# Optimization experiments

Hardware: AMD Instinct MI355X
Metric: run time of the kernel (lower is better)

Reference implementation:

```python
import jax, jax.numpy as jnp
import numpy as np

B, N, F_IN, H, K = 8, 4096, 64, 64, 3


def setup_inputs() -> dict:
    key = jax.random.key(0)
    ks = jax.random.split(key, 8)
    s_in = 1.0 / np.sqrt(F_IN * K)
    s_h = 1.0 / np.sqrt(H * K)
    return {
        "input_tensor": jax.random.normal(ks[0], (B, N, F_IN), jnp.float32),
        "graph": jax.random.normal(ks[1], (B, N, N), jnp.float32) / np.sqrt(N),
        "h_cur": jax.random.normal(ks[2], (B, N, H), jnp.float32),
        "c_cur": jax.random.normal(ks[3], (B, N, H), jnp.float32),
        "W1": jax.random.normal(ks[4], (K, F_IN, 4 * H), jnp.float32) * s_in,
        "b1": jnp.zeros((4 * H,), jnp.float32),
        "W2": jax.random.normal(ks[5], (K, H, 4 * H), jnp.float32) * s_h,
        "b2": jnp.zeros((4 * H,), jnp.float32),
        "batch_size": B,
    }


def cheb_conv(x, L, W, b):
    """Batched Chebyshev graph conv.
    x: [B,N,F], L: [B,N,N] (per-sample scaled Laplacian), W: [K,F,O], b: [O].
    T_0 = x, T_1 = L x, T_k = 2 L T_{k-1} - T_{k-2}; out = sum_k T_k W_k + b.
    """
    k_order = W.shape[0]  # static
    t_km2 = x
    out = jnp.einsum("bnf,fo->bno", t_km2, W[0])
    if k_order > 1:
        t_km1 = jnp.einsum("bmn,bnf->bmf", L, x)
        out = out + jnp.einsum("bnf,fo->bno", t_km1, W[1])
        for k in range(2, k_order):
            t_k = 2.0 * jnp.einsum("bmn,bnf->bmf", L, t_km1) - t_km2
            out = out + jnp.einsum("bnf,fo->bno", t_k, W[k])
            t_km2, t_km1 = t_km1, t_k
    return out + b


def reference(input_tensor, graph, h_cur, c_cur, W1, b1, W2, b2, batch_size):
    # per-sample ChebConv on x and h (batched via einsum), then fused LSTM gates
    combined = cheb_conv(input_tensor, graph, W1, b1) + cheb_conv(h_cur, graph, W2, b2)
    hd = h_cur.shape[-1]
    cc_i, cc_f, cc_o, cc_g = jnp.split(combined, [hd, 2 * hd, 3 * hd], axis=2)
    i = jax.nn.sigmoid(cc_i)
    f = jax.nn.sigmoid(cc_f)
    o = jax.nn.sigmoid(cc_o)
    g = jnp.tanh(cc_g)
    c_next = f * c_cur + i * g
    h_next = o * jnp.tanh(c_next)
    return (h_next, c_next)
```

## Files before the change

kernel.cpp:

```cpp
#include <hip/hip_runtime.h>
#include <stdint.h>

#define BB 8
#define NN 4096
#define HH 64
#define C2 128

typedef float f32x4 __attribute__((ext_vector_type(4)));
typedef __bf16 bf16x8 __attribute__((ext_vector_type(8)));
typedef unsigned int u32x4 __attribute__((ext_vector_type(4)));

__device__ __forceinline__ unsigned short f2bf(float x) {
  unsigned int u = __float_as_uint(x);
  u += 0x7FFFu + ((u >> 16) & 1u);
  return (unsigned short)(u >> 16);
}
__device__ __forceinline__ unsigned int pack2(float a, float b) {
  return (unsigned int)f2bf(a) | ((unsigned int)f2bf(b) << 16);
}

__global__ __launch_bounds__(256) void k_prepX(const float* __restrict__ x,
                                               const float* __restrict__ h,
                                               unsigned short* __restrict__ XbfT) {
  __shared__ __align__(16) unsigned short lds[64 * 136];
  const int b = blockIdx.y;
  const int n0 = blockIdx.x * 64;
  const int t = threadIdx.x;
#pragma unroll
  for (int i = 0; i < 4; ++i) {
    int e = t + i * 256;
    int n = e >> 4, f4 = e & 15;
    size_t src = (((size_t)b * NN + n0 + n) << 6) + f4 * 4;
    f32x4 vx = *(const f32x4*)(x + src);
    f32x4 vh = *(const f32x4*)(h + src);
    unsigned short* px = &lds[n * 136 + f4 * 4];
    px[0] = f2bf(vx.x); px[1] = f2bf(vx.y); px[2] = f2bf(vx.z); px[3] = f2bf(vx.w);
    unsigned short* ph = &lds[n * 136 + 64 + f4 * 4];
    ph[0] = f2bf(vh.x); ph[1] = f2bf(vh.y); ph[2] = f2bf(vh.z); ph[3] = f2bf(vh.w);
  }
  __syncthreads();
  const int f2 = t >> 1, half = t & 1;
  unsigned int w[16];
#pragma unroll
  for (int i = 0; i < 16; ++i) {
    int na = half * 32 + i * 2;
    w[i] = (unsigned int)lds[na * 136 + f2] | ((unsigned int)lds[(na + 1) * 136 + f2] << 16);
  }
  size_t off = ((size_t)b * C2 + f2) * NN + n0 + half * 32;
  u32x4* dst = (u32x4*)(XbfT + off);
  u32x4 v0 = {w[0], w[1], w[2], w[3]};   dst[0] = v0;
  u32x4 v1 = {w[4], w[5], w[6], w[7]};   dst[1] = v1;
  u32x4 v2 = {w[8], w[9], w[10], w[11]}; dst[2] = v2;
  u32x4 v3 = {w[12], w[13], w[14], w[15]}; dst[3] = v3;
}

__global__ __launch_bounds__(256) void k_prepW(const float* __restrict__ W1,
                                               const float* __restrict__ W2,
                                               unsigned short* __restrict__ WcatT) {
  int tid = blockIdx.x * 256 + threadIdx.x;
  int o = tid & 255;
  int kk = (tid >> 8) * 2;
  unsigned int out = 0;
#pragma unroll
  for (int j = 0; j < 2; ++j) {
    int k = kk + j;
    int kb = k >> 6, f = k & 63;
    const float* src = (kb & 1) ? W2 : W1;
    float v = src[(((kb >> 1) * 64 + f) << 8) + o];
    out |= ((unsigned int)f2bf(v)) << (16 * j);
  }
  *(unsigned int*)(WcatT + (size_t)o * 384 + kk) = out;
}

template <int PASS>
__global__ __launch_bounds__(256) void k_gemmL(
    const float* __restrict__ L, const unsigned short* __restrict__ Rt,
    unsigned short* __restrict__ T1row, unsigned short* __restrict__ T1T,
    unsigned short* __restrict__ T2row,
    const float* __restrict__ x, const float* __restrict__ h) {
  __shared__ __align__(16) unsigned short Ab[2][64 * 72];
  __shared__ __align__(16) unsigned short Bbuf[2][128 * 64];
  const int b = blockIdx.y;
  const int n0 = blockIdx.x * 64;
  const int t = threadIdx.x;
  const int w = t >> 6, l = t & 63;
  const int wr = w >> 1, wc = w & 1;
  const int l15 = l & 15, l4 = l >> 4;

  const float* Lb = L + ((size_t)b * NN + n0) * NN;
  const unsigned short* Rb = Rt + (size_t)b * C2 * NN;

  f32x4 areg[2][4];
  u32x4 breg[4];
  f32x4 acc[2][4];
  f32x4 z = {0.f, 0.f, 0.f, 0.f};
#pragma unroll
  for (int i = 0; i < 2; ++i)
#pragma unroll
    for (int j = 0; j < 4; ++j) acc[i][j] = z;

#define LOAD_A(kt, ar)                                                     \
  {                                                                        \
    int k0 = (kt) * 64;                                                    \
    _Pragma("unroll") for (int i = 0; i < 4; ++i) {                        \
      int e = t + i * 256; int row = e >> 4, c4 = e & 15;                  \
      (ar)[i] = *(const f32x4*)(Lb + (size_t)row * NN + k0 + c4 * 4);      \
    }                                                                      \
  }
#define LOAD_B(kt, br)                                                     \
  {                                                                        \
    int k0 = (kt) * 64;                                                    \
    _Pragma("unroll") for (int i = 0; i < 4; ++i) {                        \
      int e = t + i * 256; int c = e >> 3, q = e & 7;                      \
      (br)[i] = *(const u32x4*)(Rb + (size_t)c * NN + k0 + q * 8);         \
    }                                                                      \
  }
#define STORE_A(p, ar)                                                     \
  {                                                                        \
    _Pragma("unroll") for (int i = 0; i < 4; ++i) {                        \
      int e = t + i * 256; int row = e >> 4, c4 = e & 15;                  \
      *(uint2*)&Ab[p][row * 72 + c4 * 4] =                                 \
          make_uint2(pack2((ar)[i].x, (ar)[i].y), pack2((ar)[i].z, (ar)[i].w)); \
    }                                                                      \
  }
#define STORE_B(p, br)                                                     \
  {                                                                        \
    _Pragma("unroll") for (int i = 0; i < 4; ++i) {                        \
      int e = t + i * 256; int c = e >> 3, q = e & 7;                      \
      int ks = (q * 8) ^ ((c & 7) << 3);                                   \
      *(u32x4*)&Bbuf[p][c * 64 + ks] = (br)[i];                            \
    }                                                                      \
  }

  LOAD_A(0, areg[0]);
  LOAD_B(0, breg);
  STORE_A(0, areg[0]);
  STORE_B(0, breg);
  LOAD_A(1, areg[1]);
  __syncthreads();

  const int NT = NN / 64;
  for (int kt = 0; kt < NT; ++kt) {
    const int p = kt & 1;
    if (kt + 2 < NT) LOAD_A(kt + 2, areg[p]);
    if (kt + 1 < NT) LOAD_B(kt + 1, breg);

    bf16x8 af[2][2], bfr[4][2];
#pragma unroll
    for (int rf = 0; rf < 2; ++rf)
#pragma unroll
      for (int ks = 0; ks < 2; ++ks) {
        int n = wr * 32 + rf * 16 + l15;
        af[rf][ks] = *(const bf16x8*)&Ab[p][n * 72 + ks * 32 + l4 * 8];
      }
#pragma unroll
    for (int cf = 0; cf < 4; ++cf)
#pragma unroll
      for (int ks = 0; ks < 2; ++ks) {
        int c = wc * 64 + cf * 16 + l15;
        int kk = (ks * 32 + l4 * 8) ^ ((c & 7) << 3);
        bfr[cf][ks] = *(const bf16x8*)&Bbuf[p][c * 64 + kk];
      }
#pragma unroll
    for (int ks = 0; ks < 2; ++ks)
#pragma unroll
      for (int rf = 0; rf < 2; ++rf)
#pragma unroll
        for (int cf = 0; cf < 4; ++cf)
          acc[rf][cf] = __builtin_amdgcn_mfma_f32_16x16x32_bf16(
              af[rf][ks], bfr[cf][ks], acc[rf][cf], 0, 0, 0);

    if (kt + 1 < NT) {
      STORE_A(p ^ 1, areg[(kt + 1) & 1]);
      STORE_B(p ^ 1, breg);
    }
    __syncthreads();
  }

#pragma unroll
  for (int rf = 0; rf < 2; ++rf)
#pragma unroll
    for (int cf = 0; cf < 4; ++cf) {
      int c = wc * 64 + cf * 16 + l15;
      int nb = n0 + wr * 32 + rf * 16 + l4 * 4;
      f32x4 v = acc[rf][cf];
      if (PASS == 1) {
#pragma unroll
        for (int r = 0; r < 4; ++r)
          T1row[((size_t)b * NN + nb + r) * C2 + c] = f2bf(v[r]);
        *(uint2*)(T1T + ((size_t)b * C2 + c) * NN + nb) =
            make_uint2(pack2(v[0], v[1]), pack2(v[2], v[3]));
      } else {
#pragma unroll
        for (int r = 0; r < 4; ++r) {
          int n = nb + r;
          float t0 = (c < 64) ? x[(((size_t)b * NN + n) << 6) + c]
                              : h[(((size_t)b * NN + n) << 6) + (c - 64)];
          T2row[((size_t)b * NN + n) * C2 + c] = f2bf(2.0f * v[r] - t0);
        }
      }
    }
#undef LOAD_A
#undef LOAD_B
#undef STORE_A
#undef STORE_B
}

__global__ __launch_bounds__(256) void k_final(
    const float* __restrict__ x, const float* __restrict__ h,
    const unsigned short* __restrict__ T1row, const unsigned short* __restrict__ T2row,
    const unsigned short* __restrict__ WcatT,
    const float* __restrict__ b1, const float* __restrict__ b2,
    const float* __restrict__ c_cur, float* __restrict__ out) {
  __shared__ __align__(16) unsigned short Al[64 * 40];
  __shared__ __align__(16) unsigned short Bl[256 * 40];
  const int t = threadIdx.x;
  const int w = t >> 6, l = t & 63;
  const int l15 = l & 15, l4 = l >> 4;
  const int gr0 = blockIdx.x * 64;
  const int b = gr0 >> 12, n0 = gr0 & (NN - 1);

  f32x4 acc[16];
  f32x4 z = {0.f, 0.f, 0.f, 0.f};
#pragma unroll
  for (int i = 0; i < 16; ++i) acc[i] = z;

  for (int kt = 0; kt < 12; ++kt) {
    const int sb = kt >> 1;
    const int cb = (kt & 1) * 32;
    __syncthreads();
    if (sb < 2) {
      const float* src = (sb == 0) ? x : h;
#pragma unroll
      for (int i = 0; i < 2; ++i) {
        int e = t + i * 256; int n = e >> 3, q = e & 7;
        f32x4 v = *(const f32x4*)(src + (((size_t)b * NN + n0 + n) << 6) + cb + q * 4);
        *(uint2*)&Al[n * 40 + q * 4] = make_uint2(pack2(v.x, v.y), pack2(v.z, v.w));
      }
    } else {
      const unsigned short* src = (sb < 4) ? T1row : T2row;
      int c0 = ((sb & 1) ? 64 : 0) + cb;
      int n = t >> 2, q = t & 3;
      u32x4 v = *(const u32x4*)(src + ((size_t)b * NN + n0 + n) * C2 + c0 + q * 8);
      *(u32x4*)&Al[n * 40 + q * 8] = v;
    }
    {
      int o0 = t >> 2, q = t & 3;
#pragma unroll
      for (int i = 0; i < 4; ++i) {
        int o = o0 + i * 64;
        u32x4 v = *(const u32x4*)(WcatT + (size_t)o * 384 + kt * 32 + q * 8);
        *(u32x4*)&Bl[o * 40 + q * 8] = v;
      }
    }
    __syncthreads();
    bf16x8 afr = *(const bf16x8*)&Al[(w * 16 + l15) * 40 + l4 * 8];
#pragma unroll
    for (int cf = 0; cf < 16; ++cf) {
      bf16x8 bfr = *(const bf16x8*)&Bl[(cf * 16 + l15) * 40 + l4 * 8];
      acc[cf] = __builtin_amdgcn_mfma_f32_16x16x32_bf16(afr, bfr, acc[cf], 0, 0, 0);
    }
  }

  const int nrow = n0 + w * 16 + l4 * 4;
#pragma unroll
  for (int cf = 0; cf < 4; ++cf) {
    int j = cf * 16 + l15;
    float bi = b1[j] + b2[j];
    float bf_ = b1[64 + j] + b2[64 + j];
    float bo = b1[128 + j] + b2[128 + j];
    float bg = b1[192 + j] + b2[192 + j];
#pragma unroll
    for (int r = 0; r < 4; ++r) {
      int n = nrow + r;
      size_t base = ((size_t)b * NN + n) * HH + j;
      float ii = acc[cf][r] + bi;
      float ff = acc[cf + 4][r] + bf_;
      float oo = acc[cf + 8][r] + bo;
      float gg = acc[cf + 12][r] + bg;
      ii = 1.0f / (1.0f + __expf(-ii));
      ff = 1.0f / (1.0f + __expf(-ff));
      oo = 1.0f / (1.0f + __expf(-oo));
      gg = tanhf(gg);
      float cn = ff * c_cur[base] + ii * gg;
      float hn = oo * tanhf(cn);
      out[base] = hn;
      out[(size_t)BB * NN * HH + base] = cn;
    }
  }
}

extern "C" void kernel_launch(void* const* d_in, const int* in_sizes, int n_in,
                              void* d_out, int out_size, void* d_ws, size_t ws_size,
                              hipStream_t stream) {
  const float* x  = (const float*)d_in[0];
  const float* L  = (const float*)d_in[1];
  const float* h  = (const float*)d_in[2];
  const float* c  = (const float*)d_in[3];
  const float* W1 = (const float*)d_in[4];
  const float* b1 = (const float*)d_in[5];
  const float* W2 = (const float*)d_in[6];
  const float* b2 = (const float*)d_in[7];
  char* ws = (char*)d_ws;
  unsigned short* XbfT  = (unsigned short*)(ws);
  unsigned short* T1row = (unsigned short*)(ws + (size_t)(8u << 20));
  unsigned short* T1T   = (unsigned short*)(ws + (size_t)(16u << 20));
  unsigned short* T2row = (unsigned short*)(ws + (size_t)(24u << 20));
  unsigned short* WcatT = (unsigned short*)(ws + (size_t)(32u << 20));
  float* out = (float*)d_out;

  k_prepX<<<dim3(64, 8), 256, 0, stream>>>(x, h, XbfT);
  k_prepW<<<dim3(192), 256, 0, stream>>>(W1, W2, WcatT);
  k_gemmL<1><<<dim3(64, 8), 256, 0, stream>>>(L, XbfT, T1row, T1T, nullptr, x, h);
  k_gemmL<2><<<dim3(64, 8), 256, 0, stream>>>(L, T1T, nullptr, nullptr, T2row, x, h);
  k_final<<<dim3(512), 256, 0, stream>>>(x, h, T1row, T2row, WcatT, b1, b2, c, out);
}
```

Baseline: 1.037 ms.

## Stream L via direct global-to-LDS loads, read B from global, unify feature buffer

The L-GEMM now stages fp32 L tiles straight into LDS with global_load_lds and a swizzled layout, converting to bf16 only when fragments are built. B fragments are read from global/L2 directly instead of being staged in LDS. Blocks grow to 512 threads (8 waves, 16 rows each) and block indices are interleaved across batches. Features x, h, T1 and T2 are written into one concatenated bf16 row buffer, so the final kernel reads it without LDS staging or a loop over separate sources. This is meant to cut LDS traffic and register staging in the bandwidth-bound L pass, at the cost of fp32 LDS footprint and uncached-looking global B reads.

```diff
diff --git a/kernel.cpp b/kernel.cpp
--- a/kernel.cpp
+++ b/kernel.cpp
@@ -5,6 +5,7 @@
 #define NN 4096
 #define HH 64
 #define C2 128
+#define FW 384
 
 typedef float f32x4 __attribute__((ext_vector_type(4)));
 typedef __bf16 bf16x8 __attribute__((ext_vector_type(8)));
@@ -18,10 +19,20 @@
 __device__ __forceinline__ unsigned int pack2(float a, float b) {
   return (unsigned int)f2bf(a) | ((unsigned int)f2bf(b) << 16);
 }
+__device__ __forceinline__ bf16x8 mk_frag(f32x4 a0, f32x4 a1) {
+  u32x4 u = {pack2(a0.x, a0.y), pack2(a0.z, a0.w), pack2(a1.x, a1.y), pack2(a1.z, a1.w)};
+  return __builtin_bit_cast(bf16x8, u);
+}
+__device__ __forceinline__ void gl_lds16(const float* g, float* l) {
+  __builtin_amdgcn_global_load_lds(
+      (const __attribute__((address_space(1))) unsigned int*)g,
+      (__attribute__((address_space(3))) unsigned int*)l, 16, 0, 0);
+}
 
 __global__ __launch_bounds__(256) void k_prepX(const float* __restrict__ x,
                                                const float* __restrict__ h,
-                                               unsigned short* __restrict__ XbfT) {
+                                               unsigned short* __restrict__ XbfT,
+                                               unsigned short* __restrict__ Feat) {
   __shared__ __align__(16) unsigned short lds[64 * 136];
   const int b = blockIdx.y;
   const int n0 = blockIdx.x * 64;
@@ -39,19 +50,30 @@
     ph[0] = f2bf(vh.x); ph[1] = f2bf(vh.y); ph[2] = f2bf(vh.z); ph[3] = f2bf(vh.w);
   }
   __syncthreads();
-  const int f2 = t >> 1, half = t & 1;
-  unsigned int w[16];
-#pragma unroll
-  for (int i = 0; i < 16; ++i) {
-    int na = half * 32 + i * 2;
-    w[i] = (unsigned int)lds[na * 136 + f2] | ((unsigned int)lds[(na + 1) * 136 + f2] << 16);
-  }
-  size_t off = ((size_t)b * C2 + f2) * NN + n0 + half * 32;
-  u32x4* dst = (u32x4*)(XbfT + off);
-  u32x4 v0 = {w[0], w[1], w[2], w[3]};   dst[0] = v0;
-  u32x4 v1 = {w[4], w[5], w[6], w[7]};   dst[1] = v1;
-  u32x4 v2 = {w[8], w[9], w[10], w[11]}; dst[2] = v2;
-  u32x4 v3 = {w[12], w[13], w[14], w[15]}; dst[3] = v3;
+  {
+    const int f2 = t >> 1, half = t & 1;
+    unsigned int wbuf[16];
+#pragma unroll
+    for (int i = 0; i < 16; ++i) {
+      int na = half * 32 + i * 2;
+      wbuf[i] = (unsigned int)lds[na * 136 + f2] |
+                ((unsigned int)lds[(na + 1) * 136 + f2] << 16);
+    }
+    size_t off = ((size_t)b * C2 + f2) * NN + n0 + half * 32;
+    u32x4* dst = (u32x4*)(XbfT + off);
+    u32x4 v0 = {wbuf[0], wbuf[1], wbuf[2], wbuf[3]};     dst[0] = v0;
+    u32x4 v1 = {wbuf[4], wbuf[5], wbuf[6], wbuf[7]};     dst[1] = v1;
+    u32x4 v2 = {wbuf[8], wbuf[9], wbuf[10], wbuf[11]};   dst[2] = v2;
+    u32x4 v3 = {wbuf[12], wbuf[13], wbuf[14], wbuf[15]}; dst[3] = v3;
+  }
+  {
+    int n = t >> 2, c0 = (t & 3) * 32;
+    unsigned short* fd = Feat + ((size_t)b * NN + n0 + n) * FW + c0;
+    const unsigned short* sl = &lds[n * 136 + c0];
+#pragma unroll
+    for (int i = 0; i < 4; ++i)
+      *(u32x4*)(fd + 8 * i) = *(const u32x4*)(sl + 8 * i);
+  }
 }
 
 __global__ __launch_bounds__(256) void k_prepW(const float* __restrict__ W1,
@@ -69,223 +91,145 @@
     float v = src[(((kb >> 1) * 64 + f) << 8) + o];
     out |= ((unsigned int)f2bf(v)) << (16 * j);
   }
-  *(unsigned int*)(WcatT + (size_t)o * 384 + kk) = out;
+  *(unsigned int*)(WcatT + (size_t)o * FW + kk) = out;
 }
 
 template <int PASS>
-__global__ __launch_bounds__(256) void k_gemmL(
-    const float* __restrict__ L, const unsigned short* __restrict__ Rt,
-    unsigned short* __restrict__ T1row, unsigned short* __restrict__ T1T,
-    unsigned short* __restrict__ T2row,
-    const float* __restrict__ x, const float* __restrict__ h) {
-  __shared__ __align__(16) unsigned short Ab[2][64 * 72];
-  __shared__ __align__(16) unsigned short Bbuf[2][128 * 64];
-  const int b = blockIdx.y;
-  const int n0 = blockIdx.x * 64;
+__global__ __launch_bounds__(512, 4) void k_gemmL(
+    const float* __restrict__ L, const unsigned short* __restrict__ Bpan,
+    unsigned short* __restrict__ T1T, unsigned short* __restrict__ Feat,
+    const float* __restrict__ xg, const float* __restrict__ hg) {
+  __shared__ __align__(16) float As[2][64 * 64];
+  const int blk = blockIdx.x;
+  const int b = blk & 7;
+  const int n0 = (blk >> 3) * 64;
   const int t = threadIdx.x;
   const int w = t >> 6, l = t & 63;
   const int wr = w >> 1, wc = w & 1;
   const int l15 = l & 15, l4 = l >> 4;
 
   const float* Lb = L + ((size_t)b * NN + n0) * NN;
-  const unsigned short* Rb = Rt + (size_t)b * C2 * NN;
-
-  f32x4 areg[2][4];
-  u32x4 breg[4];
-  f32x4 acc[2][4];
+  const unsigned short* Bp = Bpan + (size_t)b * C2 * NN;
+
+  f32x4 acc[4];
   f32x4 z = {0.f, 0.f, 0.f, 0.f};
 #pragma unroll
-  for (int i = 0; i < 2; ++i)
-#pragma unroll
-    for (int j = 0; j < 4; ++j) acc[i][j] = z;
-
-#define LOAD_A(kt, ar)                                                     \
-  {                                                                        \
-    int k0 = (kt) * 64;                                                    \
-    _Pragma("unroll") for (int i = 0; i < 4; ++i) {                        \
-      int e = t + i * 256; int row = e >> 4, c4 = e & 15;                  \
-      (ar)[i] = *(const f32x4*)(Lb + (size_t)row * NN + k0 + c4 * 4);      \
-    }                                                                      \
-  }
-#define LOAD_B(kt, br)                                                     \
-  {                                                                        \
-    int k0 = (kt) * 64;                                                    \
-    _Pragma("unroll") for (int i = 0; i < 4; ++i) {                        \
-      int e = t + i * 256; int c = e >> 3, q = e & 7;                      \
-      (br)[i] = *(const u32x4*)(Rb + (size_t)c * NN + k0 + q * 8);         \
-    }                                                                      \
-  }
-#define STORE_A(p, ar)                                                     \
-  {                                                                        \
-    _Pragma("unroll") for (int i = 0; i < 4; ++i) {                        \
-      int e = t + i * 256; int row = e >> 4, c4 = e & 15;                  \
-      *(uint2*)&Ab[p][row * 72 + c4 * 4] =                                 \
-          make_uint2(pack2((ar)[i].x, (ar)[i].y), pack2((ar)[i].z, (ar)[i].w)); \
-    }                                                                      \
-  }
-#define STORE_B(p, br)                                                     \
-  {                                                                        \
-    _Pragma("unroll") for (int i = 0; i < 4; ++i) {                        \
-      int e = t + i * 256; int c = e >> 3, q = e & 7;                      \
-      int ks = (q * 8) ^ ((c & 7) << 3);                                   \
-      *(u32x4*)&Bbuf[p][c * 64 + ks] = (br)[i];                            \
-    }                                                                      \
-  }
-
-  LOAD_A(0, areg[0]);
-  LOAD_B(0, breg);
-  STORE_A(0, areg[0]);
-  STORE_B(0, breg);
-  LOAD_A(1, areg[1]);
+  for (int i = 0; i < 4; ++i) acc[i] = z;
+
+#define STAGE(kt, p)                                                        \
+  {                                                                         \
+    int k0s = (kt) * 64;                                                    \
+    _Pragma("unroll") for (int i = 0; i < 2; ++i) {                         \
+      int seg = w * 2 + i;                          \
+      int r = seg * 4 + (l >> 4);                                           \
+      int s = l & 15;                                                       \
+      const float* src = Lb + (size_t)r * NN + k0s + ((s ^ (r & 15)) << 2); \
+      gl_lds16(src, &As[p][seg * 256]);                                     \
+    }                                                                       \
+  }
+
+#define COMPUTE(p, kt)                                                      \
+  {                                                                         \
+    int k0c = (kt) * 64;                                                    \
+    u32x4 br[8];                                                            \
+    _Pragma("unroll") for (int cf = 0; cf < 4; ++cf)                        \
+      _Pragma("unroll") for (int ks = 0; ks < 2; ++ks)                      \
+        br[cf * 2 + ks] = *(const u32x4*)(                                  \
+            Bp + (size_t)(wc * 64 + cf * 16 + l15) * NN + k0c + ks * 32 + l4 * 8); \
+    bf16x8 af[2];                                                           \
+    _Pragma("unroll") for (int ks = 0; ks < 2; ++ks) {                      \
+      int q = ks * 8 + l4 * 2;                                              \
+      int n = wr * 16 + l15;                             \
+      f32x4 a0 = *(const f32x4*)&As[p][n * 64 + ((q ^ l15) << 2)];          \
+      f32x4 a1 = *(const f32x4*)&As[p][n * 64 + (((q + 1) ^ l15) << 2)];    \
+      af[ks] = mk_frag(a0, a1);                                             \
+    }                                                                       \
+    _Pragma("unroll") for (int ks = 0; ks < 2; ++ks)                        \
+      _Pragma("unroll") for (int cf = 0; cf < 4; ++cf)                      \
+        acc[cf] = __builtin_amdgcn_mfma_f32_16x16x32_bf16(                  \
+            af[ks], __builtin_bit_cast(bf16x8, br[cf * 2 + ks]), acc[cf], 0, 0, 0); \
+  }
+
+  STAGE(0, 0);
   __syncthreads();
-
-  const int NT = NN / 64;
-  for (int kt = 0; kt < NT; ++kt) {
-    const int p = kt & 1;
-    if (kt + 2 < NT) LOAD_A(kt + 2, areg[p]);
-    if (kt + 1 < NT) LOAD_B(kt + 1, breg);
-
-    bf16x8 af[2][2], bfr[4][2];
-#pragma unroll
-    for (int rf = 0; rf < 2; ++rf)
-#pragma unroll
-      for (int ks = 0; ks < 2; ++ks) {
-        int n = wr * 32 + rf * 16 + l15;
-        af[rf][ks] = *(const bf16x8*)&Ab[p][n * 72 + ks * 32 + l4 * 8];
-      }
-#pragma unroll
-    for (int cf = 0; cf < 4; ++cf)
-#pragma unroll
-      for (int ks = 0; ks < 2; ++ks) {
-        int c = wc * 64 + cf * 16 + l15;
-        int kk = (ks * 32 + l4 * 8) ^ ((c & 7) << 3);
-        bfr[cf][ks] = *(const bf16x8*)&Bbuf[p][c * 64 + kk];
-      }
-#pragma unroll
-    for (int ks = 0; ks < 2; ++ks)
-#pragma unroll
-      for (int rf = 0; rf < 2; ++rf)
-#pragma unroll
-        for (int cf = 0; cf < 4; ++cf)
-          acc[rf][cf] = __builtin_amdgcn_mfma_f32_16x16x32_bf16(
-              af[rf][ks], bfr[cf][ks], acc[rf][cf], 0, 0, 0);
-
-    if (kt + 1 < NT) {
-      STORE_A(p ^ 1, areg[(kt + 1) & 1]);
-      STORE_B(p ^ 1, breg);
-    }
+#pragma unroll 1
+  for (int kt = 0; kt < NN / 64; kt += 2) {
+    STAGE(kt + 1, 1);
+    COMPUTE(0, kt);
     __syncthreads();
-  }
-
-#pragma unroll
-  for (int rf = 0; rf < 2; ++rf)
-#pragma unroll
-    for (int cf = 0; cf < 4; ++cf) {
-      int c = wc * 64 + cf * 16 + l15;
-      int nb = n0 + wr * 32 + rf * 16 + l4 * 4;
-      f32x4 v = acc[rf][cf];
-      if (PASS == 1) {
-#pragma unroll
-        for (int r = 0; r < 4; ++r)
-          T1row[((size_t)b * NN + nb + r) * C2 + c] = f2bf(v[r]);
-        *(uint2*)(T1T + ((size_t)b * C2 + c) * NN + nb) =
-            make_uint2(pack2(v[0], v[1]), pack2(v[2], v[3]));
-      } else {
-#pragma unroll
-        for (int r = 0; r < 4; ++r) {
-          int n = nb + r;
-          float t0 = (c < 64) ? x[(((size_t)b * NN + n) << 6) + c]
-                              : h[(((size_t)b * NN + n) << 6) + (c - 64)];
-          T2row[((size_t)b * NN + n) * C2 + c] = f2bf(2.0f * v[r] - t0);
-        }
-      }
-    }
-#undef LOAD_A
-#undef LOAD_B
-#undef STORE_A
-#undef STORE_B
+    if (kt + 2 < NN / 64) STAGE(kt + 2, 0);
+    COMPUTE(1, kt + 1);
+    __syncthreads();
+  }
+#undef STAGE
+#undef COMPUTE
+
+  const int nb = n0 + wr * 16 + l4 * 4;
+#pragma unroll
+  for (int cf = 0; cf < 4; ++cf) {
+    int c = wc * 64 + cf * 16 + l15;
+    f32x4 v = acc[cf];
+    if (PASS == 1) {
+      *(uint2*)(T1T + ((size_t)b * C2 + c) * NN + nb) =
+          make_uint2(pack2(v.x, v.y), pack2(v.z, v.w));
+      unsigned short* fr = Feat + ((size_t)b * NN + nb) * FW + 128 + c;
+#pragma unroll
+      for (int r = 0; r < 4; ++r) fr[(size_t)r * FW] = f2bf(v[r]);
+    } else {
+      const float* t0p = (c < 64) ? (xg + (((size_t)b * NN + nb) << 6) + c)
+                                  : (hg + (((size_t)b * NN + nb) << 6) + (c - 64));
+      unsigned short* fr = Feat + ((size_t)b * NN + nb) * FW + 256 + c;
+#pragma unroll
+      for (int r = 0; r < 4; ++r)
+        fr[(size_t)r * FW] = f2bf(2.0f * v[r] - t0p[(size_t)r << 6]);
+    }
+  }
 }
 
 __global__ __launch_bounds__(256) void k_final(
-    const float* __restrict__ x, const float* __restrict__ h,
-    const unsigned short* __restrict__ T1row, const unsigned short* __restrict__ T2row,
-    const unsigned short* __restrict__ WcatT,
+    const unsigned short* __restrict__ Feat, const unsigned short* __restrict__ WcatT,
     const float* __restrict__ b1, const float* __restrict__ b2,
     const float* __restrict__ c_cur, float* __restrict__ out) {
-  __shared__ __align__(16) unsigned short Al[64 * 40];
-  __shared__ __align__(16) unsigned short Bl[256 * 40];
-  const int t = threadIdx.x;
-  const int w = t >> 6, l = t & 63;
+  const int t = threadIdx.x, w = t >> 6, l = t & 63;
   const int l15 = l & 15, l4 = l >> 4;
-  const int gr0 = blockIdx.x * 64;
-  const int b = gr0 >> 12, n0 = gr0 & (NN - 1);
-
+  const int b = blockIdx.x >> 6;
+  const int n0 = (blockIdx.x & 63) * 64;
+  const int n = n0 + w * 16 + l15;
+
+  const unsigned short* frow = Feat + ((size_t)b * NN + n) * FW + l4 * 8;
   f32x4 acc[16];
   f32x4 z = {0.f, 0.f, 0.f, 0.f};
 #pragma unroll
   for (int i = 0; i < 16; ++i) acc[i] = z;
 
-  for (int kt = 0; kt < 12; ++kt) {
-    const int sb = kt >> 1;
-    const int cb = (kt & 1) * 32;
-    __syncthreads();
-    if (sb < 2) {
-      const float* src = (sb == 0) ? x : h;
-#pragma unroll
-      for (int i = 0; i < 2; ++i) {
-        int e = t + i * 256; int n = e >> 3, q = e & 7;
-        f32x4 v = *(const f32x4*)(src + (((size_t)b * NN + n0 + n) << 6) + cb + q * 4);
-        *(uint2*)&Al[n * 40 + q * 4] = make_uint2(pack2(v.x, v.y), pack2(v.z, v.w));
-      }
-    } else {
-      const unsigned short* src = (sb < 4) ? T1row : T2row;
-      int c0 = ((sb & 1) ? 64 : 0) + cb;
-      int n = t >> 2, q = t & 3;
-      u32x4 v = *(const u32x4*)(src + ((size_t)b * NN + n0 + n) * C2 + c0 + q * 8);
-      *(u32x4*)&Al[n * 40 + q * 8] = v;
-    }
-    {
-      int o0 = t >> 2, q = t & 3;
-#pragma unroll
-      for (int i = 0; i < 4; ++i) {
-        int o = o0 + i * 64;
-        u32x4 v = *(const u32x4*)(WcatT + (size_t)o * 384 + kt * 32 + q * 8);
-        *(u32x4*)&Bl[o * 40 + q * 8] = v;
-      }
-    }
-    __syncthreads();
-    bf16x8 afr = *(const bf16x8*)&Al[(w * 16 + l15) * 40 + l4 * 8];
-#pragma unroll
-    for (int cf = 0; cf < 16; ++cf) {
-      bf16x8 bfr = *(const bf16x8*)&Bl[(cf * 16 + l15) * 40 + l4 * 8];
-      acc[cf] = __builtin_amdgcn_mfma_f32_16x16x32_bf16(afr, bfr, acc[cf], 0, 0, 0);
-    }
-  }
-
-  const int nrow = n0 + w * 16 + l4 * 4;
-#pragma unroll
-  for (int cf = 0; cf < 4; ++cf) {
-    int j = cf * 16 + l15;
-    float bi = b1[j] + b2[j];
-    float bf_ = b1[64 + j] + b2[64 + j];
-    float bo = b1[128 + j] + b2[128 + j];
-    float bg = b1[192 + j] + b2[192 + j];
+#pragma unroll 1
+  for (int ks = 0; ks < 12; ++ks) {
+    bf16x8 bf = *(const bf16x8*)(frow + ks * 32);
+#pragma unroll
+    for (int fA = 0; fA < 16; ++fA) {
+      bf16x8 aw = *(const bf16x8*)(WcatT + (size_t)(fA * 16 + l15) * FW + ks * 32 + l4 * 8);
+      acc[fA] = __builtin_amdgcn_mfma_f32_16x16x32_bf16(aw, bf, acc[fA], 0, 0, 0);
+    }
+  }
+
+  const size_t base_n = (((size_t)b * NN + n) << 6);
+#pragma unroll
+  for (int fA = 0; fA < 4; ++fA) {
 #pragma unroll
     for (int r = 0; r < 4; ++r) {
-      int n = nrow + r;
-      size_t base = ((size_t)b * NN + n) * HH + j;
-      float ii = acc[cf][r] + bi;
-      float ff = acc[cf + 4][r] + bf_;
-      float oo = acc[cf + 8][r] + bo;
-      float gg = acc[cf + 12][r] + bg;
+      int j = fA * 16 + l4 * 4 + r;
+      float ii = acc[fA][r]      + b1[j]       + b2[j];
+      float ff = acc[fA + 4][r]  + b1[64 + j]  + b2[64 + j];
+      float oo = acc[fA + 8][r]  + b1[128 + j] + b2[128 + j];
+      float gg = acc[fA + 12][r] + b1[192 + j] + b2[192 + j];
       ii = 1.0f / (1.0f + __expf(-ii));
       ff = 1.0f / (1.0f + __expf(-ff));
       oo = 1.0f / (1.0f + __expf(-oo));
       gg = tanhf(gg);
-      float cn = ff * c_cur[base] + ii * gg;
+      float cn = ff * c_cur[base_n + j] + ii * gg;
       float hn = oo * tanhf(cn);
-      out[base] = hn;
-      out[(size_t)BB * NN * HH + base] = cn;
+      out[base_n + j] = hn;
+      out[(size_t)BB * NN * HH + base_n + j] = cn;
     }
   }
 }
@@ -303,15 +247,14 @@
   const float* b2 = (const float*)d_in[7];
   char* ws = (char*)d_ws;
   unsigned short* XbfT  = (unsigned short*)(ws);
-  unsigned short* T1row = (unsigned short*)(ws + (size_t)(8u << 20));
-  unsigned short* T1T   = (unsigned short*)(ws + (size_t)(16u << 20));
-  unsigned short* T2row = (unsigned short*)(ws + (size_t)(24u << 20));
-  unsigned short* WcatT = (unsigned short*)(ws + (size_t)(32u << 20));
+  unsigned short* T1T   = (unsigned short*)(ws + (size_t)(8u << 20));
+  unsigned short* Feat  = (unsigned short*)(ws + (size_t)(16u << 20));
+  unsigned short* WcatT = (unsigned short*)(ws + (size_t)(40u << 20));
   float* out = (float*)d_out;
 
-  k_prepX<<<dim3(64, 8), 256, 0, stream>>>(x, h, XbfT);
+  k_prepX<<<dim3(64, 8), 256, 0, stream>>>(x, h, XbfT, Feat);
   k_prepW<<<dim3(192), 256, 0, stream>>>(W1, W2, WcatT);
-  k_gemmL<1><<<dim3(64, 8), 256, 0, stream>>>(L, XbfT, T1row, T1T, nullptr, x, h);
-  k_gemmL<2><<<dim3(64, 8), 256, 0, stream>>>(L, T1T, nullptr, nullptr, T2row, x, h);
-  k_final<<<dim3(512), 256, 0, stream>>>(x, h, T1row, T2row, WcatT, b1, b2, c, out);
-}
+  k_gemmL<1><<<dim3(512), 512, 0, stream>>>(L, XbfT, T1T, Feat, nullptr, nullptr);
+  k_gemmL<2><<<dim3(512), 512, 0, stream>>>(L, T1T, nullptr, Feat, x, h);
+  k_final<<<dim3(512), 256, 0, stream>>>(Feat, WcatT, b1, b2, c, out);
+}
```

New measurement: 1.182 ms. 1.14x slower.
